# Performance work log

Measured on AMD Instinct MI355X. Metric: run time of the kernel, lower is better.

## Reference

```python
import jax, jax.numpy as jnp
import numpy as np

B, D1, D2, D3 = 4, 64, 64, 64
CIN, COUT = 32, 32
M1, M2, M3 = 8, 8, 8


def setup_inputs() -> dict:
    key = jax.random.key(0)
    k1, k2, k3 = jax.random.split(key, 3)
    x = jax.random.normal(k1, (B, D1, D2, D3, CIN), dtype=jnp.float32)
    # scale ~ random_normal initializer (stddev 0.05 default in keras)
    w_real = jax.random.normal(k2, (CIN, COUT, M1, M2, M3), dtype=jnp.float32) * 0.05
    w_imag = jax.random.normal(k3, (CIN, COUT, M1, M2, M3), dtype=jnp.float32) * 0.05
    return {"x": x, "w_real": w_real, "w_imag": w_imag}


def reference(x, w_real, w_imag):
    # tf.signal.fft3d transforms the innermost 3 dims of [B,D1,D2,D3,C]
    x_ft = jnp.fft.fftn(x.astype(jnp.complex64), axes=(2, 3, 4))
    # low-mode truncation over axes 1,2,3 (as in the original code)
    x_low = x_ft[:, :M1, :M2, :M3, :]                       # [B,M1,M2,M3,CIN]
    w = (w_real + 1j * w_imag).astype(jnp.complex64)         # [CIN,COUT,M1,M2,M3]
    x_low = jnp.transpose(x_low, (0, 4, 1, 2, 3))            # [B,CIN,M1,M2,M3]
    # Faithful to original: i,j of weights are summed out, k is matched.
    out_low = jnp.einsum('bcmnk,coijk->bomnk', x_low, w)     # [B,COUT,M1,M2,M3]
    out_low = jnp.transpose(out_low, (0, 2, 3, 4, 1))        # [B,M1,M2,M3,COUT]
    # zero-padded spectrum (replaces the wasteful tensor_scatter_nd_update)
    out_ft = jnp.zeros((B, D1, D2, D3, COUT), dtype=jnp.complex64)
    out_ft = out_ft.at[:, :M1, :M2, :M3, :].set(out_low)
    y = jnp.fft.ifftn(out_ft, axes=(2, 3, 4))
    return jnp.real(y).astype(jnp.float32)
```

## Files before the change

kernel.cpp:

```cpp
#include <hip/hip_runtime.h>


#define PI2F 6.28318530717958647692f

__device__ __forceinline__ float2 cmul(float2 a, float2 b) {
    return make_float2(a.x * b.x - a.y * b.y, a.x * b.y + a.y * b.x);
}

__global__ void k_weff(const float* __restrict__ wr, const float* __restrict__ wi,
                       float2* __restrict__ Weff) {
    int t = blockIdx.x * 256 + threadIdx.x;
    int base = (t >> 3) * 512 + (t & 7);
    float sr = 0.f, si = 0.f;
    #pragma unroll 8
    for (int ij = 0; ij < 64; ++ij) { sr += wr[base + ij * 8]; si += wi[base + ij * 8]; }
    Weff[t] = make_float2(sr, si);
}

__global__ void k_T(const float2* __restrict__ Weff, float2* __restrict__ T) {
    __shared__ float2 tw32[32];
    __shared__ float2 A[256];
    int t = threadIdx.x;
    int c = blockIdx.x;
    if (t < 32) {
        float s, co_;
        __sincosf((PI2F / 32.f) * (float)t, &s, &co_);
        tw32[t] = make_float2(co_, s);
    }
    __syncthreads();
    {
        float2 acc = make_float2(0.f, 0.f);
        for (int fc = 0; fc < 32; ++fc) {
            float2 v = Weff[fc * 256 + t];
            float2 e = tw32[(fc * c) & 31];
            acc.x += v.x * e.x + v.y * e.y;
            acc.y += v.y * e.x - v.x * e.y;
        }
        A[t] = acc;
    }
    __syncthreads();
    {
        int f3 = t >> 5, co = t & 31;
        float2 acc = make_float2(0.f, 0.f);
        for (int o = 0; o < 32; ++o) {
            float2 v = A[o * 8 + f3];
            float2 e = tw32[(o * co) & 31];
            acc.x += v.x * e.x - v.y * e.y;
            acc.y += v.x * e.y + v.y * e.x;
        }
        T[c * 256 + t] = acc;
    }
}

__global__ void k_dft_d2(const float* __restrict__ x, float2* __restrict__ S1) {
    int t = blockIdx.x * 256 + threadIdx.x;
    int c4 = t & 7;
    int d3 = (t >> 3) & 63;
    int f2 = (t >> 9) & 7;
    int d1 = (t >> 12) & 7;
    int b  = t >> 15;
    const float4* xp = (const float4*)(x + (size_t)b * 8388608 + (size_t)d1 * 131072
                                         + d3 * 32 + c4 * 4);
    float s, c;
    __sincosf((PI2F / 64.f) * (float)f2, &s, &c);
    float2 step = make_float2(c, -s);
    float2 w = make_float2(1.f, 0.f);
    float2 a0 = {0,0}, a1 = {0,0}, a2 = {0,0}, a3 = {0,0};
    for (int d2 = 0; d2 < 64; ++d2) {
        float4 v = xp[d2 * 512];
        a0.x += v.x * w.x; a0.y += v.x * w.y;
        a1.x += v.y * w.x; a1.y += v.y * w.y;
        a2.x += v.z * w.x; a2.y += v.z * w.y;
        a3.x += v.w * w.x; a3.y += v.w * w.y;
        w = cmul(w, step);
    }
    float2* sp = S1 + (size_t)(t >> 9) * 2048 + d3 * 32 + c4 * 4;
    ((float4*)sp)[0] = make_float4(a0.x, a0.y, a1.x, a1.y);
    ((float4*)sp)[1] = make_float4(a2.x, a2.y, a3.x, a3.y);
}

__global__ void k_mid(const float2* __restrict__ S1, const float2* __restrict__ T,
                      float2* __restrict__ S6) {
    __shared__ float2 lin[2048];
    __shared__ float2 ls2[256];
    __shared__ float2 ls5[256];
    __shared__ float2 tw64[64];
    int t = threadIdx.x;
    int gid = blockIdx.x;
    {
        const float4* src = (const float4*)(S1 + (size_t)gid * 2048);
        float4* dst = (float4*)lin;
        #pragma unroll
        for (int j = 0; j < 4; ++j) dst[t + j * 256] = src[t + j * 256];
    }
    if (t < 64) {
        float s, c;
        __sincosf((PI2F / 64.f) * (float)t, &s, &c);
        tw64[t] = make_float2(c, s);
    }
    __syncthreads();
    {
        int f3 = t >> 5, c = t & 31;
        float2 e = tw64[f3];
        float2 step = make_float2(e.x, -e.y);
        float2 w = make_float2(1.f, 0.f);
        float2 acc = make_float2(0.f, 0.f);
        for (int d3 = 0; d3 < 64; ++d3) {
            float2 v = lin[d3 * 32 + c];
            acc.x += v.x * w.x - v.y * w.y;
            acc.y += v.x * w.y + v.y * w.x;
            w = cmul(w, step);
        }
        ls2[f3 * 32 + c] = acc;
    }
    __syncthreads();
    {
        int f3 = t >> 5;
        float2 acc = make_float2(0.f, 0.f);
        for (int c = 0; c < 32; ++c) {
            float2 a = ls2[f3 * 32 + (c)];
            float2 w = T[c * 256 + t];
            acc.x += a.x * w.x - a.y * w.y;
            acc.y += a.x * w.y + a.y * w.x;
        }
        ls5[t] = acc;
    }
    __syncthreads();
    {
        int co = t & 31, d3r = t >> 5;
        float2* outp = S6 + (size_t)gid * 2048;
        #pragma unroll
        for (int j = 0; j < 8; ++j) {
            int d3 = d3r + 8 * j;
            float2 acc = make_float2(0.f, 0.f);
            #pragma unroll
            for (int f3 = 0; f3 < 8; ++f3) {
                float2 v = ls5[f3 * 32 + co];
                float2 e = tw64[(f3 * d3) & 63];
                acc.x += v.x * e.x - v.y * e.y;
                acc.y += v.x * e.y + v.y * e.x;
            }
            outp[d3 * 32 + co] = acc;
        }
    }
}

__global__ void k_final(const float2* __restrict__ S6, float* __restrict__ out) {
    int t4 = blockIdx.x * 256 + threadIdx.x;
    int u = t4 << 2;
    int co = u & 31;
    int d3 = (u >> 5) & 63;
    int d2 = (u >> 11) & 63;
    int d1 = (u >> 17) & 63;
    int b  = u >> 23;
    float4 r;
    if (d1 >= 8) {
        r = make_float4(0.f, 0.f, 0.f, 0.f);
    } else {
        const float2* q = S6 + (size_t)(b * 8 + d1) * 16384 + d3 * 32 + co;
        float a0 = 0.f, a1 = 0.f, a2 = 0.f, a3 = 0.f;
        #pragma unroll
        for (int f2 = 0; f2 < 8; ++f2) {
            float ang = (PI2F / 64.f) * (float)((f2 * d2) & 63);
            float s, c;
            __sincosf(ang, &s, &c);
            float2 v0 = q[f2 * 2048 + 0];
            float2 v1 = q[f2 * 2048 + 1];
            float2 v2 = q[f2 * 2048 + 2];
            float2 v3 = q[f2 * 2048 + 3];
            a0 += v0.x * c - v0.y * s;
            a1 += v1.x * c - v1.y * s;
            a2 += v2.x * c - v2.y * s;
            a3 += v3.x * c - v3.y * s;
        }
        const float sc = 1.f / 131072.f;
        r = make_float4(a0 * sc, a1 * sc, a2 * sc, a3 * sc);
    }
    ((float4*)out)[t4] = r;
}

extern "C" void kernel_launch(void* const* d_in, const int* in_sizes, int n_in,
                              void* d_out, int out_size, void* d_ws, size_t ws_size,
                              hipStream_t stream) {
    const float* x  = (const float*)d_in[0];
    const float* wr = (const float*)d_in[1];
    const float* wi = (const float*)d_in[2];
    float* out = (float*)d_out;

    float2* Weff = (float2*)d_ws;
    float2* T    = Weff + 8192;
    float2* S1   = T + 8192;
    float2* S6   = S1 + 524288;

    k_weff  <<<32,    256, 0, stream>>>(wr, wi, Weff);
    k_T     <<<32,    256, 0, stream>>>(Weff, T);
    k_dft_d2<<<512,   256, 0, stream>>>(x, S1);
    k_mid   <<<256,   256, 0, stream>>>(S1, T, S6);
    k_final <<<32768, 256, 0, stream>>>(S6, out);
}
```

Measured before the change: 238.7 us.

## Fuse d2 DFT into mid kernel and tile final inverse DFT through LDS

Folds the forward d2 DFT into the mid kernel, so each block computes its 64 d3 rows straight from x into shared memory and the S1 intermediate round trip and one launch go away. The final kernel is restructured so each block stages one slice of S6 in LDS, reads twiddles from a table instead of calling sincos per element, and reuses the staged values across 16 output rows. Output is written with nontemporal vector stores, and zero regions exit early. The mid kernel now runs only 256 blocks with more global-load work each, which may leave the x reads under-parallelized.

```diff
diff --git a/kernel.cpp b/kernel.cpp
--- a/kernel.cpp
+++ b/kernel.cpp
@@ -2,6 +2,8 @@
 
 
 #define PI2F 6.28318530717958647692f
+
+typedef float vf4 __attribute__((ext_vector_type(4)));
 
 __device__ __forceinline__ float2 cmul(float2 a, float2 b) {
     return make_float2(a.x * b.x - a.y * b.y, a.x * b.y + a.y * b.x);
@@ -52,51 +54,52 @@
     }
 }
 
-__global__ void k_dft_d2(const float* __restrict__ x, float2* __restrict__ S1) {
-    int t = blockIdx.x * 256 + threadIdx.x;
-    int c4 = t & 7;
-    int d3 = (t >> 3) & 63;
-    int f2 = (t >> 9) & 7;
-    int d1 = (t >> 12) & 7;
-    int b  = t >> 15;
-    const float4* xp = (const float4*)(x + (size_t)b * 8388608 + (size_t)d1 * 131072
-                                         + d3 * 32 + c4 * 4);
-    float s, c;
-    __sincosf((PI2F / 64.f) * (float)f2, &s, &c);
-    float2 step = make_float2(c, -s);
-    float2 w = make_float2(1.f, 0.f);
-    float2 a0 = {0,0}, a1 = {0,0}, a2 = {0,0}, a3 = {0,0};
-    for (int d2 = 0; d2 < 64; ++d2) {
-        float4 v = xp[d2 * 512];
-        a0.x += v.x * w.x; a0.y += v.x * w.y;
-        a1.x += v.y * w.x; a1.y += v.y * w.y;
-        a2.x += v.z * w.x; a2.y += v.z * w.y;
-        a3.x += v.w * w.x; a3.y += v.w * w.y;
-        w = cmul(w, step);
-    }
-    float2* sp = S1 + (size_t)(t >> 9) * 2048 + d3 * 32 + c4 * 4;
-    ((float4*)sp)[0] = make_float4(a0.x, a0.y, a1.x, a1.y);
-    ((float4*)sp)[1] = make_float4(a2.x, a2.y, a3.x, a3.y);
-}
-
-__global__ void k_mid(const float2* __restrict__ S1, const float2* __restrict__ T,
-                      float2* __restrict__ S6) {
+__global__ void k_mid2(const float* __restrict__ x, const float2* __restrict__ T,
+                       float2* __restrict__ S6) {
     __shared__ float2 lin[2048];
     __shared__ float2 ls2[256];
     __shared__ float2 ls5[256];
     __shared__ float2 tw64[64];
     int t = threadIdx.x;
     int gid = blockIdx.x;
-    {
-        const float4* src = (const float4*)(S1 + (size_t)gid * 2048);
-        float4* dst = (float4*)lin;
-        #pragma unroll
-        for (int j = 0; j < 4; ++j) dst[t + j * 256] = src[t + j * 256];
-    }
+    int f2 = gid >> 5;
+    int s  = gid & 31;
+    int b  = s >> 3, d1 = s & 7;
     if (t < 64) {
-        float s, c;
-        __sincosf((PI2F / 64.f) * (float)t, &s, &c);
-        tw64[t] = make_float2(c, s);
+        float sn, cs;
+        __sincosf((PI2F / 64.f) * (float)t, &sn, &cs);
+        tw64[t] = make_float2(cs, sn);
+    }
+    {
+        int c4 = t & 7;
+        int d3a = t >> 3;
+        const float4* pa = (const float4*)(x + (size_t)b * 8388608 + (size_t)d1 * 131072
+                                             + d3a * 32 + c4 * 4);
+        const float4* pb = pa + 256;
+        float sn, cs;
+        __sincosf((PI2F / 64.f) * (float)f2, &sn, &cs);
+        float2 step = make_float2(cs, -sn);
+        float2 w = make_float2(1.f, 0.f);
+        float2 accA0 = {0,0}, accA1 = {0,0}, accA2 = {0,0}, accA3 = {0,0};
+        float2 accB0 = {0,0}, accB1 = {0,0}, accB2 = {0,0}, accB3 = {0,0};
+        #pragma unroll 4
+        for (int d2 = 0; d2 < 64; ++d2) {
+            float4 va = pa[d2 * 512];
+            float4 vb = pb[d2 * 512];
+            accA0.x += va.x * w.x; accA0.y += va.x * w.y;
+            accA1.x += va.y * w.x; accA1.y += va.y * w.y;
+            accA2.x += va.z * w.x; accA2.y += va.z * w.y;
+            accA3.x += va.w * w.x; accA3.y += va.w * w.y;
+            accB0.x += vb.x * w.x; accB0.y += vb.x * w.y;
+            accB1.x += vb.y * w.x; accB1.y += vb.y * w.y;
+            accB2.x += vb.z * w.x; accB2.y += vb.z * w.y;
+            accB3.x += vb.w * w.x; accB3.y += vb.w * w.y;
+            w = cmul(w, step);
+        }
+        float2* la = lin + d3a * 32 + c4 * 4;
+        float2* lb = la + 1024;
+        la[0] = accA0; la[1] = accA1; la[2] = accA2; la[3] = accA3;
+        lb[0] = accB0; lb[1] = accB1; lb[2] = accB2; lb[3] = accB3;
     }
     __syncthreads();
     {
@@ -118,7 +121,7 @@
         int f3 = t >> 5;
         float2 acc = make_float2(0.f, 0.f);
         for (int c = 0; c < 32; ++c) {
-            float2 a = ls2[f3 * 32 + (c)];
+            float2 a = ls2[f3 * 32 + c];
             float2 w = T[c * 256 + t];
             acc.x += a.x * w.x - a.y * w.y;
             acc.y += a.x * w.y + a.y * w.x;
@@ -128,7 +131,7 @@
     __syncthreads();
     {
         int co = t & 31, d3r = t >> 5;
-        float2* outp = S6 + (size_t)gid * 2048;
+        float2* outp = S6 + (size_t)(s * 8 + f2) * 2048;
         #pragma unroll
         for (int j = 0; j < 8; ++j) {
             int d3 = d3r + 8 * j;
@@ -145,38 +148,67 @@
     }
 }
 
-__global__ void k_final(const float2* __restrict__ S6, float* __restrict__ out) {
-    int t4 = blockIdx.x * 256 + threadIdx.x;
-    int u = t4 << 2;
-    int co = u & 31;
-    int d3 = (u >> 5) & 63;
-    int d2 = (u >> 11) & 63;
-    int d1 = (u >> 17) & 63;
-    int b  = u >> 23;
-    float4 r;
+__global__ void k_final2(const float2* __restrict__ S6, float* __restrict__ out) {
+    __shared__ float2 ls[2048];
+    __shared__ float2 tw[64];
+    int t = threadIdx.x;
+    int gid = blockIdx.x;
+    int blk = gid & 7;
+    int d1  = (gid >> 3) & 63;
+    int b   = gid >> 9;
+    int co4 = t & 7;
+    int d3r = (t >> 3) & 7;
+    int d2q = t >> 6;
+    float* obase = out + (size_t)b * 8388608 + (size_t)d1 * 131072
+                 + (blk * 8 + d3r) * 32 + co4 * 4;
     if (d1 >= 8) {
-        r = make_float4(0.f, 0.f, 0.f, 0.f);
-    } else {
-        const float2* q = S6 + (size_t)(b * 8 + d1) * 16384 + d3 * 32 + co;
-        float a0 = 0.f, a1 = 0.f, a2 = 0.f, a3 = 0.f;
+        vf4 z = {0.f, 0.f, 0.f, 0.f};
+        #pragma unroll
+        for (int i = 0; i < 16; ++i) {
+            int d2 = d2q * 16 + i;
+            __builtin_nontemporal_store(z, (vf4*)(obase + d2 * 2048));
+        }
+        return;
+    }
+    if (t < 64) {
+        float sn, cs;
+        __sincosf((PI2F / 64.f) * (float)t, &sn, &cs);
+        tw[t] = make_float2(cs, sn);
+    }
+    {
+        const float4* src = (const float4*)(S6 + (size_t)(b * 8 + d1) * 16384);
+        float4* dst = (float4*)ls;
+        #pragma unroll
+        for (int j = 0; j < 4; ++j) {
+            int i4 = t + j * 256;
+            int f2 = i4 >> 7, rem = i4 & 127;
+            dst[i4] = src[f2 * 1024 + blk * 128 + rem];
+        }
+    }
+    __syncthreads();
+    float2 v[8][4];
+    #pragma unroll
+    for (int f2 = 0; f2 < 8; ++f2) {
+        #pragma unroll
+        for (int k = 0; k < 4; ++k)
+            v[f2][k] = ls[f2 * 256 + d3r * 32 + co4 * 4 + k];
+    }
+    const float sc = 1.f / 131072.f;
+    #pragma unroll 2
+    for (int i = 0; i < 16; ++i) {
+        int d2 = d2q * 16 + i;
+        float rx = 0.f, ry = 0.f, rz = 0.f, rw = 0.f;
         #pragma unroll
         for (int f2 = 0; f2 < 8; ++f2) {
-            float ang = (PI2F / 64.f) * (float)((f2 * d2) & 63);
-            float s, c;
-            __sincosf(ang, &s, &c);
-            float2 v0 = q[f2 * 2048 + 0];
-            float2 v1 = q[f2 * 2048 + 1];
-            float2 v2 = q[f2 * 2048 + 2];
-            float2 v3 = q[f2 * 2048 + 3];
-            a0 += v0.x * c - v0.y * s;
-            a1 += v1.x * c - v1.y * s;
-            a2 += v2.x * c - v2.y * s;
-            a3 += v3.x * c - v3.y * s;
-        }
-        const float sc = 1.f / 131072.f;
-        r = make_float4(a0 * sc, a1 * sc, a2 * sc, a3 * sc);
-    }
-    ((float4*)out)[t4] = r;
+            float2 e = tw[(f2 * d2) & 63];
+            rx += v[f2][0].x * e.x - v[f2][0].y * e.y;
+            ry += v[f2][1].x * e.x - v[f2][1].y * e.y;
+            rz += v[f2][2].x * e.x - v[f2][2].y * e.y;
+            rw += v[f2][3].x * e.x - v[f2][3].y * e.y;
+        }
+        vf4 r = {rx * sc, ry * sc, rz * sc, rw * sc};
+        __builtin_nontemporal_store(r, (vf4*)(obase + d2 * 2048));
+    }
 }
 
 extern "C" void kernel_launch(void* const* d_in, const int* in_sizes, int n_in,
@@ -189,12 +221,10 @@
 
     float2* Weff = (float2*)d_ws;
     float2* T    = Weff + 8192;
-    float2* S1   = T + 8192;
-    float2* S6   = S1 + 524288;
-
-    k_weff  <<<32,    256, 0, stream>>>(wr, wi, Weff);
-    k_T     <<<32,    256, 0, stream>>>(Weff, T);
-    k_dft_d2<<<512,   256, 0, stream>>>(x, S1);
-    k_mid   <<<256,   256, 0, stream>>>(S1, T, S6);
-    k_final <<<32768, 256, 0, stream>>>(S6, out);
-}
+    float2* S6   = T + 8192;
+
+    k_weff  <<<32,   256, 0, stream>>>(wr, wi, Weff);
+    k_T     <<<32,   256, 0, stream>>>(Weff, T);
+    k_mid2  <<<256,  256, 0, stream>>>(x, T, S6);
+    k_final2<<<2048, 256, 0, stream>>>(S6, out);
+}
```

Result: no change. 241.3 us (+1.1%).
